# Kernel tuning notes

Measured on AMD Instinct MI355X. Metric: run time of the kernel, lower is better.

Reference implementation:

```python
import jax, jax.numpy as jnp
import numpy as np

NUM_HEADS = 16
LN_EPS = 1e-5
ROPE_BASE = 10000.0


def setup_inputs() -> dict:
    key = jax.random.key(0)
    ks = jax.random.split(key, 4)
    B, T, D = 2, 2048, 1024
    return {
        "x": jax.random.normal(ks[0], (B, T, D), jnp.float32),
        "in_proj_weight": jax.random.normal(ks[1], (3 * D, D), jnp.float32) * 0.02,
        "in_proj_bias": jnp.zeros((3 * D,), jnp.float32),
        "out_proj_weight": jax.random.normal(ks[2], (D, D), jnp.float32) * 0.02,
        "out_proj_bias": jnp.zeros((D,), jnp.float32),
        "ln_gamma": jnp.ones((D,), jnp.float32),
        "ln_beta": jnp.zeros((D,), jnp.float32),
    }


def _rope_cos_sin(T, head_dim):
    # standard rotary tables; apply_rotary in the source truncates the
    # concatenated (T, head_dim) tables back to (T, head_dim//2), so we
    # build the half-width tables directly.
    inv_freq = 1.0 / (ROPE_BASE ** (jnp.arange(0, head_dim, 2, dtype=jnp.float32) / head_dim))
    t = jnp.arange(T, dtype=jnp.float32)
    freqs = jnp.outer(t, inv_freq)  # (T, head_dim//2)
    return jnp.cos(freqs), jnp.sin(freqs)


def _apply_rotary(x, cos, sin):
    # x: (B, H, T, hD), split-half rotary variant
    x1, x2 = jnp.split(x, 2, axis=-1)
    cos = cos[None, None]
    sin = sin[None, None]
    return jnp.concatenate([x1 * cos - x2 * sin, x2 * cos + x1 * sin], axis=-1).astype(x.dtype)


def reference(x, in_proj_weight, in_proj_bias, out_proj_weight, out_proj_bias, ln_gamma, ln_beta):
    B, T, D = x.shape
    H = NUM_HEADS
    hD = D // H
    residual = x

    # pre-LN
    mu = jnp.mean(x, axis=-1, keepdims=True)
    var = jnp.var(x, axis=-1, keepdims=True)
    xn = (x - mu) / jnp.sqrt(var + LN_EPS) * ln_gamma + ln_beta

    w_q, w_k, w_v = jnp.split(in_proj_weight, 3, axis=0)
    b_q, b_k, b_v = jnp.split(in_proj_bias, 3, axis=0)

    # first (manual) projection with bias
    q = xn @ w_q.T + b_q
    k = xn @ w_k.T + b_k
    v = xn @ w_v.T + b_v

    # RoPE per head
    q = q.reshape(B, T, H, hD).transpose(0, 2, 1, 3)
    k = k.reshape(B, T, H, hD).transpose(0, 2, 1, 3)
    cos, sin = _rope_cos_sin(T, hD)
    q = _apply_rotary(q, cos, sin)
    k = _apply_rotary(k, cos, sin)
    q = q.transpose(0, 2, 1, 3).reshape(B, T, D)
    k = k.transpose(0, 2, 1, 3).reshape(B, T, D)

    # second projection inside multi_head_attention_forward
    # (use_separate_proj_weight=True, in_proj_bias=None -> bias-free)
    q = q @ w_q.T
    k = k @ w_k.T
    v = v @ w_v.T

    q = q.reshape(B, T, H, hD).transpose(0, 2, 1, 3) * (hD ** -0.5)
    k = k.reshape(B, T, H, hD).transpose(0, 2, 1, 3)
    v = v.reshape(B, T, H, hD).transpose(0, 2, 1, 3)

    scores = jnp.einsum('bhtd,bhsd->bhts', q, k)
    causal = jnp.triu(jnp.full((T, T), -jnp.inf, dtype=scores.dtype), k=1)
    attn_weights = jax.nn.softmax(scores + causal, axis=-1)  # (B, H, T, T)

    out = jnp.einsum('bhts,bhsd->bhtd', attn_weights, v)
    out = out.transpose(0, 2, 1, 3).reshape(B, T, D)
    out = out @ out_proj_weight.T + out_proj_bias
    return out + residual, attn_weights
```

## Files before the change

kernel.cpp:

```cpp
#include <hip/hip_runtime.h>
#include <math.h>
#include <stdint.h>

typedef unsigned short u16;
typedef __bf16 bf16x8 __attribute__((ext_vector_type(8)));
typedef float f32x4 __attribute__((ext_vector_type(4)));

constexpr int Tq = 2048;
constexpr int D  = 1024;
constexpr int NHc = 16;
constexpr int Bc = 2;
constexpr int Mrows = Bc * Tq;

__device__ __forceinline__ float wsum(float v){
#pragma unroll
  for(int o=32;o;o>>=1) v += __shfl_xor(v,o);
  return v;
}
__device__ __forceinline__ u16 f2bf(float f){
  union{ float f; unsigned u; } v; v.f = f;
  unsigned r = v.u + 0x7fffu + ((v.u >> 16) & 1u);
  return (u16)(r >> 16);
}
__device__ __forceinline__ float bf2f(u16 b){
  union{ unsigned u; float f; } v; v.u = ((unsigned)b) << 16;
  return v.f;
}
__device__ __forceinline__ void gl2lds16(const void* g, void* l){
  __builtin_amdgcn_global_load_lds(
      (const __attribute__((address_space(1))) unsigned int*)g,
      (__attribute__((address_space(3))) unsigned int*)l, 16, 0, 0);
}

__global__ __launch_bounds__(256) void cvt_kernel(const float* __restrict__ s,
                                                  u16* __restrict__ d){
  const int i = blockIdx.x*256 + threadIdx.x;
  const float4 v = ((const float4*)s)[i];
  ushort4 o; o.x=f2bf(v.x); o.y=f2bf(v.y); o.z=f2bf(v.z); o.w=f2bf(v.w);
  ((ushort4*)d)[i] = o;
}

__global__ __launch_bounds__(256) void ln_kernel(const float* __restrict__ x,
    const float* __restrict__ g, const float* __restrict__ b,
    u16* __restrict__ xn){
  const int row = blockIdx.x;
  const int tid = threadIdx.x;
  const float4 v = ((const float4*)(x + (size_t)row*D))[tid];
  float s = v.x+v.y+v.z+v.w;
  float q = v.x*v.x+v.y*v.y+v.z*v.z+v.w*v.w;
  s = wsum(s); q = wsum(q);
  __shared__ float sb[4], qb[4];
  if((tid&63)==0){ sb[tid>>6]=s; qb[tid>>6]=q; }
  __syncthreads();
  const float ts = sb[0]+sb[1]+sb[2]+sb[3];
  const float tq = qb[0]+qb[1]+qb[2]+qb[3];
  const float mu   = ts*(1.0f/D);
  const float var  = tq*(1.0f/D) - mu*mu;
  const float rstd = rsqrtf(var + 1e-5f);
  const float4 gv = ((const float4*)g)[tid];
  const float4 bv = ((const float4*)b)[tid];
  ushort4 o;
  o.x = f2bf((v.x-mu)*rstd*gv.x + bv.x);
  o.y = f2bf((v.y-mu)*rstd*gv.y + bv.y);
  o.z = f2bf((v.z-mu)*rstd*gv.z + bv.z);
  o.w = f2bf((v.w-mu)*rstd*gv.w + bv.w);
  ((ushort4*)(xn + (size_t)row*D))[tid] = o;
}

__global__ __launch_bounds__(256) void rope_tab_kernel(float2* __restrict__ tab){
  const int idx = blockIdx.x*256 + threadIdx.x;
  const int t = idx >> 5, fi = idx & 31;
  const float inv = powf(10000.0f, -(float)fi*(1.0f/32.0f));
  const float ang = (float)t * inv;
  tab[idx] = make_float2(cosf(ang), sinf(ang));
}

__global__ __launch_bounds__(256) void gemm_qkv1(
    const u16* __restrict__ A, const u16* __restrict__ B,
    const float* __restrict__ bias, const float2* __restrict__ tab,
    u16* __restrict__ out){
  __shared__ __align__(16) u16 As[128*32];
  __shared__ __align__(16) u16 Bs[128*32];
  const int tid  = threadIdx.x;
  const int lane = tid & 63, wv = tid >> 6;
  const int wRow = (wv >> 1) * 64, wCol = (wv & 1) * 64;
  const int mBase = blockIdx.y*128, nBase = blockIdx.x*128;
  const int quad = lane >> 4, r16 = lane & 15;
  const int sRow = lane >> 2;
  const int sCol = (lane & 3) * 8;
  const char* smemA = (const char*)As;
  const char* smemB = (const char*)Bs;

  f32x4 acc[4][4];
#pragma unroll
  for(int i=0;i<4;i++)
#pragma unroll
    for(int j=0;j<4;j++) acc[i][j] = (f32x4)(0.f);

  for(int k0=0;k0<D;k0+=32){
#pragma unroll
    for(int rdn=0;rdn<2;rdn++){
      const int row = rdn*64 + wv*16 + sRow;
      gl2lds16(A + (size_t)(mBase + row)*D + k0 + sCol,
               (void*)((char*)As + rdn*4096 + wv*1024));
      gl2lds16(B + (size_t)(nBase + row)*D + k0 + sCol,
               (void*)((char*)Bs + rdn*4096 + wv*1024));
    }
    __syncthreads();
    bf16x8 af[4], bfr[4];
#pragma unroll
    for(int i=0;i<4;i++)
      af[i]  = *(const bf16x8*)(smemA + (wRow + i*16 + r16)*64 + quad*16);
#pragma unroll
    for(int j=0;j<4;j++)
      bfr[j] = *(const bf16x8*)(smemB + (wCol + j*16 + r16)*64 + quad*16);
#pragma unroll
    for(int i=0;i<4;i++)
#pragma unroll
      for(int j=0;j<4;j++)
        acc[i][j] = __builtin_amdgcn_mfma_f32_16x16x32_bf16(af[i], bfr[j], acc[i][j], 0,0,0);
    __syncthreads();
  }

  const int sel  = nBase >> 10;
  const int nLoc = nBase & 1023;
  u16* C = out + (size_t)sel*Mrows*D;
  if(sel < 2){
#pragma unroll
    for(int i=0;i<4;i++){
#pragma unroll
      for(int jp=0;jp<2;jp++){
        const int hp  = jp*16 + r16;
        const int col = nLoc + wCol + hp;
        const float bv0 = bias[nBase + wCol + hp];
        const float bv1 = bias[nBase + wCol + hp + 32];
#pragma unroll
        for(int reg=0;reg<4;reg++){
          const int mm = mBase + wRow + i*16 + quad*4 + reg;
          const float2 cs = tab[((mm & (Tq-1))<<5) + hp];
          const float a0 = acc[i][jp][reg]   + bv0;
          const float a1 = acc[i][jp+2][reg] + bv1;
          C[(size_t)mm*D + col]      = f2bf(a0*cs.x - a1*cs.y);
          C[(size_t)mm*D + col + 32] = f2bf(a1*cs.x + a0*cs.y);
        }
      }
    }
  } else {
#pragma unroll
    for(int i=0;i<4;i++){
#pragma unroll
      for(int j=0;j<4;j++){
        const int n = nBase + wCol + j*16 + r16;
        const float bv = bias[n];
        const int col = nLoc + wCol + j*16 + r16;
#pragma unroll
        for(int reg=0;reg<4;reg++){
          const int mm = mBase + wRow + i*16 + quad*4 + reg;
          C[(size_t)mm*D + col] = f2bf(acc[i][j][reg] + bv);
        }
      }
    }
  }
}

__global__ __launch_bounds__(256) void gemm_stack3(
    const u16* __restrict__ A, const u16* __restrict__ Bw,
    u16* __restrict__ C){
  __shared__ __align__(16) u16 As[128*32];
  __shared__ __align__(16) u16 Bs[128*32];
  const int wsel = blockIdx.y >> 5;
  const u16* B = Bw + (size_t)wsel*D*D;
  const int tid  = threadIdx.x;
  const int lane = tid & 63, wv = tid >> 6;
  const int wRow = (wv >> 1) * 64, wCol = (wv & 1) * 64;
  const int mBase = blockIdx.y*128, nBase = blockIdx.x*128;
  const int quad = lane >> 4, r16 = lane & 15;
  const int sRow = lane >> 2;
  const int sCol = (lane & 3) * 8;
  const char* smemA = (const char*)As;
  const char* smemB = (const char*)Bs;

  f32x4 acc[4][4];
#pragma unroll
  for(int i=0;i<4;i++)
#pragma unroll
    for(int j=0;j<4;j++) acc[i][j] = (f32x4)(0.f);

  for(int k0=0;k0<D;k0+=32){
#pragma unroll
    for(int rdn=0;rdn<2;rdn++){
      const int row = rdn*64 + wv*16 + sRow;
      gl2lds16(A + (size_t)(mBase + row)*D + k0 + sCol,
               (void*)((char*)As + rdn*4096 + wv*1024));
      gl2lds16(B + (size_t)(nBase + row)*D + k0 + sCol,
               (void*)((char*)Bs + rdn*4096 + wv*1024));
    }
    __syncthreads();
    bf16x8 af[4], bfr[4];
#pragma unroll
    for(int i=0;i<4;i++)
      af[i]  = *(const bf16x8*)(smemA + (wRow + i*16 + r16)*64 + quad*16);
#pragma unroll
    for(int j=0;j<4;j++)
      bfr[j] = *(const bf16x8*)(smemB + (wCol + j*16 + r16)*64 + quad*16);
#pragma unroll
    for(int i=0;i<4;i++)
#pragma unroll
      for(int j=0;j<4;j++)
        acc[i][j] = __builtin_amdgcn_mfma_f32_16x16x32_bf16(af[i], bfr[j], acc[i][j], 0,0,0);
    __syncthreads();
  }

#pragma unroll
  for(int i=0;i<4;i++){
#pragma unroll
    for(int j=0;j<4;j++){
      const int n = nBase + wCol + j*16 + r16;
#pragma unroll
      for(int reg=0;reg<4;reg++){
        const int mm = mBase + wRow + i*16 + quad*4 + reg;
        C[(size_t)mm*D + n] = f2bf(acc[i][j][reg]);
      }
    }
  }
}

__global__ __launch_bounds__(256) void gemm_out(
    const u16* __restrict__ A, const u16* __restrict__ B, float* __restrict__ C,
    const float* __restrict__ bias, const float* __restrict__ resid){
  __shared__ __align__(16) u16 As[128*32];
  __shared__ __align__(16) u16 Bs[128*32];
  const int tid  = threadIdx.x;
  const int lane = tid & 63, wv = tid >> 6;
  const int wRow = (wv >> 1) * 64, wCol = (wv & 1) * 64;
  const int mBase = blockIdx.y*128, nBase = blockIdx.x*128;
  const int quad = lane >> 4, r16 = lane & 15;
  const int sRow = lane >> 2;
  const int sCol = (lane & 3) * 8;
  const char* smemA = (const char*)As;
  const char* smemB = (const char*)Bs;

  f32x4 acc[4][4];
#pragma unroll
  for(int i=0;i<4;i++)
#pragma unroll
    for(int j=0;j<4;j++) acc[i][j] = (f32x4)(0.f);

  for(int k0=0;k0<D;k0+=32){
#pragma unroll
    for(int rdn=0;rdn<2;rdn++){
      const int row = rdn*64 + wv*16 + sRow;
      gl2lds16(A + (size_t)(mBase + row)*D + k0 + sCol,
               (void*)((char*)As + rdn*4096 + wv*1024));
      gl2lds16(B + (size_t)(nBase + row)*D + k0 + sCol,
               (void*)((char*)Bs + rdn*4096 + wv*1024));
    }
    __syncthreads();
    bf16x8 af[4], bfr[4];
#pragma unroll
    for(int i=0;i<4;i++)
      af[i]  = *(const bf16x8*)(smemA + (wRow + i*16 + r16)*64 + quad*16);
#pragma unroll
    for(int j=0;j<4;j++)
      bfr[j] = *(const bf16x8*)(smemB + (wCol + j*16 + r16)*64 + quad*16);
#pragma unroll
    for(int i=0;i<4;i++)
#pragma unroll
      for(int j=0;j<4;j++)
        acc[i][j] = __builtin_amdgcn_mfma_f32_16x16x32_bf16(af[i], bfr[j], acc[i][j], 0,0,0);
    __syncthreads();
  }

#pragma unroll
  for(int i=0;i<4;i++){
#pragma unroll
    for(int j=0;j<4;j++){
      const int n = nBase + wCol + j*16 + r16;
      const float bv = bias[n];
#pragma unroll
      for(int reg=0;reg<4;reg++){
        const int mm = mBase + wRow + i*16 + quad*4 + reg;
        C[(size_t)mm*D + n] = acc[i][j][reg] + bv + resid[(size_t)mm*D + n];
      }
    }
  }
}

__global__ __launch_bounds__(256) void transpose_v(const u16* __restrict__ v2,
                                                   u16* __restrict__ Vt){
  __shared__ u16 tile[64][65];
  const int bt = blockIdx.x;
  const int bh = blockIdx.y;
  const int b = bh >> 4, h = bh & 15;
  const int tid = threadIdx.x;
  const int t0 = bt*64;
#pragma unroll
  for(int rep=0;rep<4;rep++){
    const int tl = rep*16 + (tid>>4);
    const int dl = (tid&15)*4;
    const ushort4 val = *(const ushort4*)(v2 + (size_t)((size_t)b*Tq + t0 + tl)*D + h*64 + dl);
    tile[tl][dl+0]=val.x; tile[tl][dl+1]=val.y; tile[tl][dl+2]=val.z; tile[tl][dl+3]=val.w;
  }
  __syncthreads();
#pragma unroll
  for(int rep=0;rep<4;rep++){
    const int dl = rep*16 + (tid>>4);
    const int tl = (tid&15)*4;
    ushort4 o;
    o.x=tile[tl+0][dl]; o.y=tile[tl+1][dl]; o.z=tile[tl+2][dl]; o.w=tile[tl+3][dl];
    *(ushort4*)(Vt + ((size_t)bh*64 + dl)*Tq + t0 + tl) = o;
  }
}

__global__ __launch_bounds__(256, 2) void attn_fused(
    const u16* __restrict__ q2, const u16* __restrict__ k2,
    const u16* __restrict__ Vt, float* __restrict__ attnW,
    u16* __restrict__ O){
  constexpr int PSS = 40;
  __shared__ __align__(16) u16 Ks[2*128*32];
  __shared__ __align__(16) u16 Vs[4*64*32];
  __shared__ __align__(16) u16 QPs[2*128*32];

  const int n    = blockIdx.x + 16*blockIdx.y;
  const int t0c  = (n >> 3) & 15;
  const int tRow = ((n >> 8) & 1) ? (15 - t0c) : t0c;
  const int bh   = (n & 7) + 8*(n >> 7);
  const int b = bh >> 4, h = bh & 15;
  const int tid = threadIdx.x, lane = tid & 63, w = tid >> 6;
  const int quad = lane >> 4, r16 = lane & 15;
  const u16* Qg = q2 + ((size_t)b*Tq + (size_t)tRow*128)*D + h*64;
  const u16* Kg = k2 + ((size_t)b*Tq)*D + h*64;
  const u16* Vg = Vt + (size_t)bh*64*Tq;
  float* Wg = attnW + (size_t)bh*Tq*Tq + (size_t)tRow*128*Tq;

  for(int ct2 = tRow+1; ct2 < Tq/128; ++ct2){
#pragma unroll
    for(int it=0; it<16; ++it){
      const int r = it*8 + (tid>>5);
      ((f32x4*)(Wg + (size_t)r*Tq + ct2*128))[tid & 31] = (f32x4)(0.f);
    }
  }

#pragma unroll
  for(int rep=0; rep<4; ++rep){
    const int kb = rep*4 + w;
    const int kk = kb >> 3, row = (kb&7)*16 + (lane>>2);
    gl2lds16(Qg + (size_t)row*D + kk*32 + (lane&3)*8,
             (void*)((char*)QPs + kb*1024));
  }
  __syncthreads();
  bf16x8 af[2][2];
#pragma unroll
  for(int i=0;i<2;i++)
#pragma unroll
    for(int kk=0;kk<2;kk++)
      af[i][kk] = *(const bf16x8*)((const char*)QPs + kk*8192
                    + (w*32 + i*16 + r16)*64 + quad*16);

  float m[2][4], l[2][4];
#pragma unroll
  for(int i=0;i<2;i++)
#pragma unroll
    for(int rg=0;rg<4;rg++){ m[i][rg] = -1e30f; l[i][rg] = 0.f; }

  for(int ct=0; ct<=tRow; ++ct){
#pragma unroll
    for(int rep=0; rep<4; ++rep){
      const int kb = rep*4 + w;
      const int kk = kb >> 3, row = (kb&7)*16 + (lane>>2);
      gl2lds16(Kg + ((size_t)ct*128 + row)*D + kk*32 + (lane&3)*8,
               (void*)((char*)Ks + kb*1024));
    }
    __syncthreads();
    f32x4 acc[2][8];
#pragma unroll
    for(int i=0;i<2;i++)
#pragma unroll
      for(int j=0;j<8;j++) acc[i][j] = (f32x4)(0.f);
#pragma unroll
    for(int kk=0;kk<2;kk++){
#pragma unroll
      for(int j=0;j<8;j++){
        const bf16x8 bfj = *(const bf16x8*)((const char*)Ks + kk*8192
                             + (j*16 + r16)*64 + quad*16);
#pragma unroll
        for(int i=0;i<2;i++)
          acc[i][j] = __builtin_amdgcn_mfma_f32_16x16x32_bf16(af[i][kk], bfj, acc[i][j],0,0,0);
      }
    }
    const bool diag = (ct == tRow);
#pragma unroll
    for(int i=0;i<2;i++){
#pragma unroll
      for(int rg=0; rg<4; ++rg){
        const int rowg = w*32 + i*16 + quad*4 + rg;
        float sv[8]; float mx = -1e30f;
#pragma unroll
        for(int j=0;j<8;j++){
          float s = acc[i][j][rg]*0.125f;
          if(diag && (j*16 + r16) > rowg) s = -1e30f;
          sv[j]=s; mx = fmaxf(mx,s);
        }
#pragma unroll
        for(int o=8;o;o>>=1) mx = fmaxf(mx, __shfl_xor(mx,o));
        const float mn = fmaxf(m[i][rg], mx);
        float ls = 0.f;
#pragma unroll
        for(int j=0;j<8;j++) ls += __expf(sv[j]-mn);
#pragma unroll
        for(int o=8;o;o>>=1) ls += __shfl_xor(ls,o);
        l[i][rg] = l[i][rg]*__expf(m[i][rg]-mn) + ls;
        m[i][rg] = mn;
      }
    }
    __syncthreads();
  }

  float rinv[2][4];
#pragma unroll
  for(int i=0;i<2;i++)
#pragma unroll
    for(int rg=0;rg<4;rg++) rinv[i][rg] = 1.0f / l[i][rg];
  f32x4 oacc[2][4];
#pragma unroll
  for(int i=0;i<2;i++)
#pragma unroll
    for(int j=0;j<4;j++) oacc[i][j] = (f32x4)(0.f);

  char* psb = (char*)QPs + w*(32*PSS*2);

  for(int ct=0; ct<=tRow; ++ct){
#pragma unroll
    for(int rep=0; rep<4; ++rep){
      const int kb = rep*4 + w;
      const int kk = kb >> 3, row = (kb&7)*16 + (lane>>2);
      gl2lds16(Kg + ((size_t)ct*128 + row)*D + kk*32 + (lane&3)*8,
               (void*)((char*)Ks + kb*1024));
      const int vrow = w*16 + (lane>>2);
      gl2lds16(Vg + (size_t)vrow*Tq + ct*128 + rep*32 + (lane&3)*8,
               (void*)((char*)Vs + (rep*4 + w)*1024));
    }
    __syncthreads();
    f32x4 acc[2][8];
#pragma unroll
    for(int i=0;i<2;i++)
#pragma unroll
      for(int j=0;j<8;j++) acc[i][j] = (f32x4)(0.f);
#pragma unroll
    for(int kk=0;kk<2;kk++){
#pragma unroll
      for(int j=0;j<8;j++){
        const bf16x8 bfj = *(const bf16x8*)((const char*)Ks + kk*8192
                             + (j*16 + r16)*64 + quad*16);
#pragma unroll
        for(int i=0;i<2;i++)
          acc[i][j] = __builtin_amdgcn_mfma_f32_16x16x32_bf16(af[i][kk], bfj, acc[i][j],0,0,0);
      }
    }
    const bool diag = (ct == tRow);
#pragma unroll
    for(int c=0;c<4;c++){
#pragma unroll
      for(int i=0;i<2;i++){
#pragma unroll
        for(int jj=0;jj<2;jj++){
          const int j = c*2 + jj;
#pragma unroll
          for(int rg=0;rg<4;rg++){
            const int rowl = i*16 + quad*4 + rg;
            const int rowg = w*32 + rowl;
            float s = acc[i][j][rg]*0.125f;
            if(diag && (j*16 + r16) > rowg) s = -1e30f;
            const float p = __expf(s - m[i][rg]) * rinv[i][rg];
            Wg[(size_t)rowg*Tq + ct*128 + j*16 + r16] = p;
            *(u16*)(psb + rowl*(PSS*2) + (jj*16 + r16)*2) = f2bf(p);
          }
        }
      }
      asm volatile("s_waitcnt lgkmcnt(0)" ::: "memory");
      __builtin_amdgcn_sched_barrier(0);
      bf16x8 pa[2];
#pragma unroll
      for(int i=0;i<2;i++)
        pa[i] = *(const bf16x8*)(psb + (i*16 + r16)*(PSS*2) + quad*16);
#pragma unroll
      for(int j2=0;j2<4;j2++){
        const bf16x8 bv = *(const bf16x8*)((const char*)Vs + c*4096
                            + (j2*16 + r16)*64 + quad*16);
        oacc[0][j2] = __builtin_amdgcn_mfma_f32_16x16x32_bf16(pa[0], bv, oacc[0][j2],0,0,0);
        oacc[1][j2] = __builtin_amdgcn_mfma_f32_16x16x32_bf16(pa[1], bv, oacc[1][j2],0,0,0);
      }
      asm volatile("s_waitcnt lgkmcnt(0)" ::: "memory");
      __builtin_amdgcn_sched_barrier(0);
    }
    __syncthreads();
  }

#pragma unroll
  for(int i=0;i<2;i++)
#pragma unroll
    for(int j2=0;j2<4;j2++)
#pragma unroll
      for(int rg=0;rg<4;rg++){
        const int trow = tRow*128 + w*32 + i*16 + quad*4 + rg;
        O[((size_t)b*Tq + trow)*D + h*64 + j2*16 + r16] = f2bf(oacc[i][j2][rg]);
      }
}

extern "C" void kernel_launch(void* const* d_in, const int* in_sizes, int n_in,
                              void* d_out, int out_size, void* d_ws, size_t ws_size,
                              hipStream_t stream){
  const float* x    = (const float*)d_in[0];
  const float* Win  = (const float*)d_in[1];
  const float* bin  = (const float*)d_in[2];
  const float* Wout = (const float*)d_in[3];
  const float* bout = (const float*)d_in[4];
  const float* gam  = (const float*)d_in[5];
  const float* bet  = (const float*)d_in[6];

  float* out   = (float*)d_out;
  float* attnW = out + (size_t)Mrows*D;

  const size_t MB = 1u<<20;
  char* ws = (char*)d_ws;
  u16* Winb  = (u16*)(ws + 0);
  u16* Woutb = (u16*)(ws + 6*MB);
  u16* xn    = (u16*)(ws + 8*MB);
  u16* Vt    = xn;
  u16* qkv1  = (u16*)(ws + 16*MB);
  u16* Oat   = qkv1;
  u16* qkv2  = (u16*)(ws + 40*MB);
  float2* tab = (float2*)(ws + 40*MB);

  const size_t DD = (size_t)D*D;
  const u16* q2 = qkv2;
  const u16* k2 = qkv2 + (size_t)Mrows*D;
  const u16* v2 = qkv2 + 2*(size_t)Mrows*D;

  cvt_kernel<<<(3*DD/4)/256, 256, 0, stream>>>(Win, Winb);
  cvt_kernel<<<(DD/4)/256, 256, 0, stream>>>(Wout, Woutb);
  rope_tab_kernel<<<(Tq*32)/256, 256, 0, stream>>>(tab);

  ln_kernel<<<Mrows, 256, 0, stream>>>(x, gam, bet, xn);

  gemm_qkv1<<<dim3(3*D/128, Mrows/128), 256, 0, stream>>>(xn, Winb, bin, tab, qkv1);

  gemm_stack3<<<dim3(D/128, 3*Mrows/128), 256, 0, stream>>>(qkv1, Winb, qkv2);

  transpose_v<<<dim3(Tq/64, Bc*NHc), 256, 0, stream>>>(v2, Vt);

  attn_fused<<<dim3(Tq/128, Bc*NHc), 256, 0, stream>>>(q2, k2, Vt, attnW, Oat);

  gemm_out<<<dim3(D/128, Mrows/128), 256, 0, stream>>>(Oat, Woutb, out, bout, x);
}
```

Measured before the change: 798.6 us.

## Merge prep kernels into one launch and write transposed V from GEMM epilogue

The two weight-conversion launches, the rope-table launch and the layernorm launch are folded into one prep kernel that dispatches on block index. The separate V transpose kernel is removed: the stacked second-projection GEMM now writes its V slice straight into the transposed [bh, d, t] layout using 4-element vector stores along t. This cuts launch overhead and one read/write pass over V, in exchange for scattered strided stores in the GEMM epilogue. A hazard to check is that Vt aliases xn, which the earlier GEMM has already finished reading.

```diff
diff --git a/kernel.cpp b/kernel.cpp
--- a/kernel.cpp
+++ b/kernel.cpp
@@ -32,19 +32,32 @@
       (__attribute__((address_space(3))) unsigned int*)l, 16, 0, 0);
 }
 
-__global__ __launch_bounds__(256) void cvt_kernel(const float* __restrict__ s,
-                                                  u16* __restrict__ d){
-  const int i = blockIdx.x*256 + threadIdx.x;
-  const float4 v = ((const float4*)s)[i];
-  ushort4 o; o.x=f2bf(v.x); o.y=f2bf(v.y); o.z=f2bf(v.z); o.w=f2bf(v.w);
-  ((ushort4*)d)[i] = o;
-}
-
-__global__ __launch_bounds__(256) void ln_kernel(const float* __restrict__ x,
-    const float* __restrict__ g, const float* __restrict__ b,
-    u16* __restrict__ xn){
-  const int row = blockIdx.x;
+__global__ __launch_bounds__(256) void prep_kernel(
+    const float* __restrict__ Win,  u16* __restrict__ Winb,
+    const float* __restrict__ Wout, u16* __restrict__ Woutb,
+    float2* __restrict__ tab,
+    const float* __restrict__ x, const float* __restrict__ g,
+    const float* __restrict__ b, u16* __restrict__ xn){
+  const int bid = blockIdx.x;
   const int tid = threadIdx.x;
+  if(bid < 4096){
+    const float* s = (bid < 3072) ? Win  : Wout;
+    u16*         d = (bid < 3072) ? Winb : Woutb;
+    const int i = (bid < 3072 ? bid : bid-3072)*256 + tid;
+    const float4 v = ((const float4*)s)[i];
+    ushort4 o; o.x=f2bf(v.x); o.y=f2bf(v.y); o.z=f2bf(v.z); o.w=f2bf(v.w);
+    ((ushort4*)d)[i] = o;
+    return;
+  }
+  if(bid < 4352){
+    const int idx = (bid-4096)*256 + tid;
+    const int t = idx >> 5, fi = idx & 31;
+    const float inv = powf(10000.0f, -(float)fi*(1.0f/32.0f));
+    const float ang = (float)t * inv;
+    tab[idx] = make_float2(cosf(ang), sinf(ang));
+    return;
+  }
+  const int row = bid - 4352;
   const float4 v = ((const float4*)(x + (size_t)row*D))[tid];
   float s = v.x+v.y+v.z+v.w;
   float q = v.x*v.x+v.y*v.y+v.z*v.z+v.w*v.w;
@@ -67,14 +80,6 @@
   ((ushort4*)(xn + (size_t)row*D))[tid] = o;
 }
 
-__global__ __launch_bounds__(256) void rope_tab_kernel(float2* __restrict__ tab){
-  const int idx = blockIdx.x*256 + threadIdx.x;
-  const int t = idx >> 5, fi = idx & 31;
-  const float inv = powf(10000.0f, -(float)fi*(1.0f/32.0f));
-  const float ang = (float)t * inv;
-  tab[idx] = make_float2(cosf(ang), sinf(ang));
-}
-
 __global__ __launch_bounds__(256) void gemm_qkv1(
     const u16* __restrict__ A, const u16* __restrict__ B,
     const float* __restrict__ bias, const float2* __restrict__ tab,
@@ -165,7 +170,7 @@
 
 __global__ __launch_bounds__(256) void gemm_stack3(
     const u16* __restrict__ A, const u16* __restrict__ Bw,
-    u16* __restrict__ C){
+    u16* __restrict__ C, u16* __restrict__ Vt){
   __shared__ __align__(16) u16 As[128*32];
   __shared__ __align__(16) u16 Bs[128*32];
   const int wsel = blockIdx.y >> 5;
@@ -211,15 +216,32 @@
     __syncthreads();
   }
 
-#pragma unroll
-  for(int i=0;i<4;i++){
-#pragma unroll
-    for(int j=0;j<4;j++){
-      const int n = nBase + wCol + j*16 + r16;
-#pragma unroll
-      for(int reg=0;reg<4;reg++){
-        const int mm = mBase + wRow + i*16 + quad*4 + reg;
-        C[(size_t)mm*D + n] = f2bf(acc[i][j][reg]);
+  if(wsel < 2){
+#pragma unroll
+    for(int i=0;i<4;i++){
+#pragma unroll
+      for(int j=0;j<4;j++){
+        const int n = nBase + wCol + j*16 + r16;
+#pragma unroll
+        for(int reg=0;reg<4;reg++){
+          const int mm = mBase + wRow + i*16 + quad*4 + reg;
+          C[(size_t)mm*D + n] = f2bf(acc[i][j][reg]);
+        }
+      }
+    }
+  } else {
+#pragma unroll
+    for(int i=0;i<4;i++){
+#pragma unroll
+      for(int j=0;j<4;j++){
+        const int n = nBase + wCol + j*16 + r16;
+        const int h = n >> 6, dloc = n & 63;
+        const int mv = (mBase - 64*128) + wRow + i*16 + quad*4;
+        const int b = mv >> 11, t = mv & (Tq-1);
+        ushort4 o;
+        o.x = f2bf(acc[i][j][0]); o.y = f2bf(acc[i][j][1]);
+        o.z = f2bf(acc[i][j][2]); o.w = f2bf(acc[i][j][3]);
+        *(ushort4*)(Vt + ((size_t)(b*16+h)*64 + dloc)*Tq + t) = o;
       }
     }
   }
@@ -286,32 +308,6 @@
   }
 }
 
-__global__ __launch_bounds__(256) void transpose_v(const u16* __restrict__ v2,
-                                                   u16* __restrict__ Vt){
-  __shared__ u16 tile[64][65];
-  const int bt = blockIdx.x;
-  const int bh = blockIdx.y;
-  const int b = bh >> 4, h = bh & 15;
-  const int tid = threadIdx.x;
-  const int t0 = bt*64;
-#pragma unroll
-  for(int rep=0;rep<4;rep++){
-    const int tl = rep*16 + (tid>>4);
-    const int dl = (tid&15)*4;
-    const ushort4 val = *(const ushort4*)(v2 + (size_t)((size_t)b*Tq + t0 + tl)*D + h*64 + dl);
-    tile[tl][dl+0]=val.x; tile[tl][dl+1]=val.y; tile[tl][dl+2]=val.z; tile[tl][dl+3]=val.w;
-  }
-  __syncthreads();
-#pragma unroll
-  for(int rep=0;rep<4;rep++){
-    const int dl = rep*16 + (tid>>4);
-    const int tl = (tid&15)*4;
-    ushort4 o;
-    o.x=tile[tl+0][dl]; o.y=tile[tl+1][dl]; o.z=tile[tl+2][dl]; o.w=tile[tl+3][dl];
-    *(ushort4*)(Vt + ((size_t)bh*64 + dl)*Tq + t0 + tl) = o;
-  }
-}
-
 __global__ __launch_bounds__(256, 2) void attn_fused(
     const u16* __restrict__ q2, const u16* __restrict__ k2,
     const u16* __restrict__ Vt, float* __restrict__ attnW,
@@ -532,22 +528,15 @@
   u16* qkv2  = (u16*)(ws + 40*MB);
   float2* tab = (float2*)(ws + 40*MB);
 
-  const size_t DD = (size_t)D*D;
   const u16* q2 = qkv2;
   const u16* k2 = qkv2 + (size_t)Mrows*D;
-  const u16* v2 = qkv2 + 2*(size_t)Mrows*D;
-
-  cvt_kernel<<<(3*DD/4)/256, 256, 0, stream>>>(Win, Winb);
-  cvt_kernel<<<(DD/4)/256, 256, 0, stream>>>(Wout, Woutb);
-  rope_tab_kernel<<<(Tq*32)/256, 256, 0, stream>>>(tab);
-
-  ln_kernel<<<Mrows, 256, 0, stream>>>(x, gam, bet, xn);
+
+  prep_kernel<<<8448, 256, 0, stream>>>(Win, Winb, Wout, Woutb, tab,
+                                        x, gam, bet, xn);
 
   gemm_qkv1<<<dim3(3*D/128, Mrows/128), 256, 0, stream>>>(xn, Winb, bin, tab, qkv1);
 
-  gemm_stack3<<<dim3(D/128, 3*Mrows/128), 256, 0, stream>>>(qkv1, Winb, qkv2);
-
-  transpose_v<<<dim3(Tq/64, Bc*NHc), 256, 0, stream>>>(v2, Vt);
+  gemm_stack3<<<dim3(D/128, 3*Mrows/128), 256, 0, stream>>>(qkv1, Winb, qkv2, Vt);
 
   attn_fused<<<dim3(Tq/128, Bc*NHc), 256, 0, stream>>>(q2, k2, Vt, attnW, Oat);
 
```

Measured after the change: 797.2 us. Within noise of the previous version (-0.2%).
